# Kernel optimization log

Measured on AMD Instinct MI355X. Metric: run time of the kernel, lower is better.

Reference implementation:

```python
import jax, jax.numpy as jnp
import numpy as np

EPS = 1e-8  # torch F.cosine_similarity default eps


def setup_inputs() -> dict:
    key = jax.random.key(0)
    ks = jax.random.split(key, 8)
    B, N, D, H = 2, 256, 256, 8
    LEN = 2 * D + 4  # flag == 1
    query = jax.random.normal(ks[0], (B, N, N, D), dtype=jnp.float32)
    k_in = jax.random.normal(ks[1], (B, N, N, D), dtype=jnp.float32)
    s_query = jax.random.uniform(ks[2], (B, N, N, 2), dtype=jnp.float32)
    s_key = jax.random.uniform(ks[3], (B, N, N, 2), dtype=jnp.float32)
    roi_mask = jnp.ones((B, N, N), dtype=jnp.float32)
    # nn.Linear(LEN, H) params
    bound = 1.0 / np.sqrt(LEN)
    W = jax.random.uniform(ks[4], (H, LEN), minval=-bound, maxval=bound, dtype=jnp.float32)
    b_lin = jax.random.uniform(ks[5], (H,), minval=-bound, maxval=bound, dtype=jnp.float32)
    return {"query": query, "key": k_in, "s_query": s_query, "s_key": s_key,
            "roi_mask": roi_mask, "W": W, "b_lin": b_lin, "node_num": 32}


def reference(query, key, s_query, s_key, roi_mask, W, b_lin, node_num):
    B, N, _, D = query.shape
    # spatial feature for flag==1: simple concat
    spat = jnp.concatenate([s_query, s_key], axis=3)          # (B,N,N,4)
    ft = jnp.concatenate([query, key, spat], axis=3)          # (B,N,N,2D+4)
    attn1 = jax.nn.sigmoid(jnp.einsum('bqkc,hc->bqkh', ft, W) + b_lin)  # (B,N,N,H)

    # cosine-similarity scores over channel dim, then relu (Attention_4)
    qn = jnp.maximum(jnp.sqrt(jnp.sum(query * query, axis=3)), EPS)
    kn = jnp.maximum(jnp.sqrt(jnp.sum(key * key, axis=3)), EPS)
    scores = jnp.sum(query * key, axis=3) / (qn * kn)         # (B,N,N)
    attn = jax.nn.relu(scores)

    # torch: values, idces = topk(attn(B,N,N,1), node_num, dim=2);
    #        atten_mask[:, :, idces, :] = 1.0
    # Fancy indexing with the full idces tensor sets dim-2 position p to 1
    # for ALL (b, row) whenever p appears ANYWHERE in idces -> a global
    # indicator vector along dim 2.
    _, idces = jax.lax.top_k(attn, node_num)                  # (B,N,node_num)
    ind = jnp.zeros((N,), dtype=attn1.dtype).at[idces.reshape(-1)].set(1.0)

    out = attn1 * roi_mask[:, :, :, None] * ind[None, None, :, None]
    return out
```

## Files before the change

kernel.cpp:

```cpp
#include <hip/hip_runtime.h>

#define NPAIR 131072
#define NDIM  256
#define NH    8
#define NN    256
#define NROWS 512
#define LEN   516
#define EPSV  1e-8f

__device__ __forceinline__ float dot4(float4 a, float4 b) {
    return fmaf(a.x, b.x, fmaf(a.y, b.y, fmaf(a.z, b.z, a.w * b.w)));
}

__global__ __launch_bounds__(64) void fused_main(
    const float* __restrict__ Q, const float* __restrict__ K,
    const float* __restrict__ SQ, const float* __restrict__ SK,
    const float* __restrict__ ROI, const float* __restrict__ W,
    const float* __restrict__ Bb, float* __restrict__ out,
    float* __restrict__ scores)
{
    __shared__ float4 ldsQ[512];
    __shared__ float4 ldsK[512];

    const int lane = threadIdx.x;
    const int p0 = blockIdx.x * 64;
    const int rsub = lane >> 3;
    const int jcol = lane & 7;

    const float4* Q4 = (const float4*)Q;
    const float4* K4 = (const float4*)K;

    float acc[11];
#pragma unroll
    for (int i = 0; i < 11; ++i) acc[i] = 0.0f;

    float4 gq[8], gk[8];
#pragma unroll
    for (int t = 0; t < 8; ++t) {
        const int r = rsub + 8 * t;
        gq[t] = Q4[(size_t)(p0 + r) * 64 + jcol];
        gk[t] = K4[(size_t)(p0 + r) * 64 + jcol];
    }

    for (int c = 0; c < 8; ++c) {
        __syncthreads();
#pragma unroll
        for (int t = 0; t < 8; ++t) {
            const int r = rsub + 8 * t;
            const int a = r * 8 + (jcol ^ rsub);
            ldsQ[a] = gq[t];
            ldsK[a] = gk[t];
        }
        if (c < 7) {
#pragma unroll
            for (int t = 0; t < 8; ++t) {
                const int r = rsub + 8 * t;
                gq[t] = Q4[(size_t)(p0 + r) * 64 + (c + 1) * 8 + jcol];
                gk[t] = K4[(size_t)(p0 + r) * 64 + (c + 1) * 8 + jcol];
            }
        }
        __syncthreads();

        float4 qc[8], kc[8];
#pragma unroll
        for (int j = 0; j < 8; ++j) {
            const int a = lane * 8 + (j ^ (lane & 7));
            qc[j] = ldsQ[a];
            kc[j] = ldsK[a];
        }

#pragma unroll
        for (int j = 0; j < 8; ++j) {
            acc[8]  += dot4(qc[j], kc[j]);
            acc[9]  += dot4(qc[j], qc[j]);
            acc[10] += dot4(kc[j], kc[j]);
        }
#pragma unroll
        for (int h = 0; h < NH; ++h) {
            const float4* wq = (const float4*)(W + h * LEN + c * 32);
            const float4* wk = (const float4*)(W + h * LEN + 256 + c * 32);
            float a0 = 0.0f;
#pragma unroll
            for (int j = 0; j < 8; ++j) {
                a0 += dot4(qc[j], wq[j]);
                a0 += dot4(kc[j], wk[j]);
            }
            acc[h] += a0;
        }
    }

    const int p = p0 + lane;
    const float qn = fmaxf(sqrtf(acc[9]),  EPSV);
    const float kn = fmaxf(sqrtf(acc[10]), EPSV);
    scores[p] = fmaxf(acc[8] / (qn * kn), 0.0f);

    const float2 sq = ((const float2*)SQ)[p];
    const float2 sk = ((const float2*)SK)[p];
    const float roi = ROI[p];
    float ov[NH];
#pragma unroll
    for (int h = 0; h < NH; ++h) {
        const float4 wt = *(const float4*)(W + h * LEN + 512);
        float x = acc[h] + sq.x * wt.x + sq.y * wt.y
                         + sk.x * wt.z + sk.y * wt.w + Bb[h];
        ov[h] = roi / (1.0f + __expf(-x));
    }
    ((float4*)out)[(size_t)p * 2]     = make_float4(ov[0], ov[1], ov[2], ov[3]);
    ((float4*)out)[(size_t)p * 2 + 1] = make_float4(ov[4], ov[5], ov[6], ov[7]);
}

__global__ void zero_ind(float* __restrict__ ind) {
    ind[threadIdx.x] = 0.0f;
}

__global__ __launch_bounds__(64) void topk_kernel(
    const float* __restrict__ scores, float* __restrict__ ind,
    const int* __restrict__ node_num)
{
    const int row = blockIdx.x;
    const int lane = threadIdx.x;
    const float4 v4 = *(const float4*)(scores + row * NN + lane * 4);
    float v[4] = {v4.x, v4.y, v4.z, v4.w};

    int Kk = node_num[0];
    if (Kk > NN) Kk = NN;
    for (int t = 0; t < Kk; t++) {
        float mv = v[0];
        int mi = lane * 4;
#pragma unroll
        for (int j = 1; j < 4; j++) {
            if (v[j] > mv) { mv = v[j]; mi = lane * 4 + j; }
        }
        for (int off = 32; off > 0; off >>= 1) {
            const float ov = __shfl_xor(mv, off, 64);
            const int   oi = __shfl_xor(mi, off, 64);
            if (ov > mv || (ov == mv && oi < mi)) { mv = ov; mi = oi; }
        }
        if (lane == 0) ind[mi] = 1.0f;
        if ((mi >> 2) == lane) v[mi & 3] = -1.0f;
    }
}

__global__ __launch_bounds__(256) void apply_ind_kernel(
    float* __restrict__ out, const float* __restrict__ ind)
{
    const int i = blockIdx.x * blockDim.x + threadIdx.x;
    float4 v = ((float4*)out)[i];
    const float m = ind[(i >> 1) & (NN - 1)];
    v.x *= m; v.y *= m; v.z *= m; v.w *= m;
    ((float4*)out)[i] = v;
}

extern "C" void kernel_launch(void* const* d_in, const int* in_sizes, int n_in,
                              void* d_out, int out_size, void* d_ws, size_t ws_size,
                              hipStream_t stream)
{
    const float* Q   = (const float*)d_in[0];
    const float* K   = (const float*)d_in[1];
    const float* SQ  = (const float*)d_in[2];
    const float* SK  = (const float*)d_in[3];
    const float* ROI = (const float*)d_in[4];
    const float* W   = (const float*)d_in[5];
    const float* Bb  = (const float*)d_in[6];
    const int* node_num = (const int*)d_in[7];

    float* out = (float*)d_out;
    float* scores = (float*)d_ws;
    float* ind = scores + NPAIR;

    fused_main<<<NPAIR / 64, 64, 0, stream>>>(Q, K, SQ, SK, ROI, W, Bb, out, scores);
    zero_ind<<<1, 256, 0, stream>>>(ind);
    topk_kernel<<<NROWS, 64, 0, stream>>>(scores, ind, node_num);
    apply_ind_kernel<<<out_size / 4 / 256, 256, 0, stream>>>(out, ind);
}
```

Before: 382.3 us.

## Use 256-thread blocks with per-wave LDS tiles and wave barriers

Main kernel now runs four independent waves per 256-thread block. Each wave owns a private LDS transpose tile, so block-wide __syncthreads are replaced by wave barriers. Chunk width is halved (16 floats per step, 16 steps) to shrink prefetch registers and raise occupancy. The cost is more loop iterations and narrower 64-byte row segments per global load, which may reduce coalescing efficiency.

```diff
diff --git a/kernel.cpp b/kernel.cpp
--- a/kernel.cpp
+++ b/kernel.cpp
@@ -12,21 +12,24 @@
     return fmaf(a.x, b.x, fmaf(a.y, b.y, fmaf(a.z, b.z, a.w * b.w)));
 }
 
-__global__ __launch_bounds__(64) void fused_main(
+__global__ __launch_bounds__(256, 4) void fused_main(
     const float* __restrict__ Q, const float* __restrict__ K,
     const float* __restrict__ SQ, const float* __restrict__ SK,
     const float* __restrict__ ROI, const float* __restrict__ W,
     const float* __restrict__ Bb, float* __restrict__ out,
     float* __restrict__ scores)
 {
-    __shared__ float4 ldsQ[512];
-    __shared__ float4 ldsK[512];
+    __shared__ float4 lds[4][2][256];
 
-    const int lane = threadIdx.x;
-    const int p0 = blockIdx.x * 64;
-    const int rsub = lane >> 3;
-    const int jcol = lane & 7;
+    const int tid  = threadIdx.x;
+    const int w    = tid >> 6;
+    const int lane = tid & 63;
+    const int p0   = blockIdx.x * 256 + w * 64;
+    const int rlo  = lane >> 2;
+    const int jc   = lane & 3;
 
+    float4* Qb = lds[w][0];
+    float4* Kb = lds[w][1];
     const float4* Q4 = (const float4*)Q;
     const float4* K4 = (const float4*)K;
 
@@ -34,54 +37,55 @@
 #pragma unroll
     for (int i = 0; i < 11; ++i) acc[i] = 0.0f;
 
-    float4 gq[8], gk[8];
+    float4 gq[4], gk[4];
 #pragma unroll
-    for (int t = 0; t < 8; ++t) {
-        const int r = rsub + 8 * t;
-        gq[t] = Q4[(size_t)(p0 + r) * 64 + jcol];
-        gk[t] = K4[(size_t)(p0 + r) * 64 + jcol];
+    for (int t = 0; t < 4; ++t) {
+        const size_t g = (size_t)(p0 + 16 * t + rlo) * 64 + jc;
+        gq[t] = Q4[g];
+        gk[t] = K4[g];
     }
 
-    for (int c = 0; c < 8; ++c) {
-        __syncthreads();
+    for (int c = 0; c < 16; ++c) {
 #pragma unroll
-        for (int t = 0; t < 8; ++t) {
-            const int r = rsub + 8 * t;
-            const int a = r * 8 + (jcol ^ rsub);
-            ldsQ[a] = gq[t];
-            ldsK[a] = gk[t];
+        for (int t = 0; t < 4; ++t) {
+            const int row = 16 * t + rlo;
+            const int idx = row * 4 + (jc ^ ((row >> 2) & 3));
+            Qb[idx] = gq[t];
+            Kb[idx] = gk[t];
         }
-        if (c < 7) {
+        if (c < 15) {
 #pragma unroll
-            for (int t = 0; t < 8; ++t) {
-                const int r = rsub + 8 * t;
-                gq[t] = Q4[(size_t)(p0 + r) * 64 + (c + 1) * 8 + jcol];
-                gk[t] = K4[(size_t)(p0 + r) * 64 + (c + 1) * 8 + jcol];
+            for (int t = 0; t < 4; ++t) {
+                const size_t g = (size_t)(p0 + 16 * t + rlo) * 64
+                               + (c + 1) * 4 + jc;
+                gq[t] = Q4[g];
+                gk[t] = K4[g];
             }
         }
-        __syncthreads();
+        __builtin_amdgcn_wave_barrier();
 
-        float4 qc[8], kc[8];
+        float4 qc[4], kc[4];
 #pragma unroll
-        for (int j = 0; j < 8; ++j) {
-            const int a = lane * 8 + (j ^ (lane & 7));
-            qc[j] = ldsQ[a];
-            kc[j] = ldsK[a];
+        for (int j = 0; j < 4; ++j) {
+            const int idx = lane * 4 + (j ^ ((lane >> 2) & 3));
+            qc[j] = Qb[idx];
+            kc[j] = Kb[idx];
         }
+        __builtin_amdgcn_wave_barrier();
 
 #pragma unroll
-        for (int j = 0; j < 8; ++j) {
+        for (int j = 0; j < 4; ++j) {
             acc[8]  += dot4(qc[j], kc[j]);
             acc[9]  += dot4(qc[j], qc[j]);
             acc[10] += dot4(kc[j], kc[j]);
         }
 #pragma unroll
         for (int h = 0; h < NH; ++h) {
-            const float4* wq = (const float4*)(W + h * LEN + c * 32);
-            const float4* wk = (const float4*)(W + h * LEN + 256 + c * 32);
+            const float4* wq = (const float4*)(W + h * LEN + c * 16);
+            const float4* wk = (const float4*)(W + h * LEN + 256 + c * 16);
             float a0 = 0.0f;
 #pragma unroll
-            for (int j = 0; j < 8; ++j) {
+            for (int j = 0; j < 4; ++j) {
                 a0 += dot4(qc[j], wq[j]);
                 a0 += dot4(kc[j], wk[j]);
             }
@@ -168,7 +172,7 @@
     float* scores = (float*)d_ws;
     float* ind = scores + NPAIR;
 
-    fused_main<<<NPAIR / 64, 64, 0, stream>>>(Q, K, SQ, SK, ROI, W, Bb, out, scores);
+    fused_main<<<NPAIR / 256, 256, 0, stream>>>(Q, K, SQ, SK, ROI, W, Bb, out, scores);
     zero_ind<<<1, 256, 0, stream>>>(ind);
     topk_kernel<<<NROWS, 64, 0, stream>>>(scores, ind, node_num);
     apply_ind_kernel<<<out_size / 4 / 256, 256, 0, stream>>>(out, ind);
```

Result: slower. 441.4 us (+15.4%).
